# Performance work log

Hardware: AMD Instinct MI355X
Metric: run time of the kernel (lower is better)

Reference implementation:

```python
import jax, jax.numpy as jnp
import numpy as np

DIM = 2048; KV_RANK = 512; Q_RANK = 768; H = 16
D_NR = 128; D_R = 64; D_V = 128
B = 8; L = 32; MAX_T = 4096; START = MAX_T - L
QK_DIM = D_NR + D_R
SCALE = 1.0 / float(np.sqrt(QK_DIM))
EPS = 1.1920929e-07  # torch.finfo(float32).eps (nn.RMSNorm default)
ROPE_BASE = 10000.0


def rms_norm(x, w):
    return x * jax.lax.rsqrt(jnp.mean(x * x, axis=-1, keepdims=True) + EPS) * w


def apply_rope(x, cos, sin):
    # x: (b, l, h, d) with d even; cos/sin: (l, d//2) -> complex multiply on pairs
    b, l, h, d = x.shape
    xp = x.reshape(b, l, h, d // 2, 2)
    xr, xi = xp[..., 0], xp[..., 1]
    c = cos[None, :, None, :]
    s = sin[None, :, None, :]
    return jnp.stack([xr * c - xi * s, xr * s + xi * c], axis=-1).reshape(b, l, h, d)


def setup_inputs() -> dict:
    key = jax.random.key(0)
    ks = jax.random.split(key, 9)
    w = 0.02
    # rotary angles for absolute positions START..START+L-1
    inv_freq = 1.0 / (ROPE_BASE ** (np.arange(0, D_R, 2, dtype=np.float32) / D_R))  # (32,)
    pos = np.arange(START, START + L, dtype=np.float32)
    ang = pos[:, None] * inv_freq[None, :]  # (L, 32)
    # causal mask over full cache: query i sits at absolute position START+i
    t = jnp.arange(MAX_T)[None, :]
    qpos = START + jnp.arange(L)[:, None]
    mask = jnp.where(t <= qpos, 0.0, -1e30).astype(jnp.float32)  # (L, MAX_T)
    return {
        "x": jax.random.normal(ks[0], (B, L, DIM), dtype=jnp.float32),
        "start_pos": START,
        "freq_cos": jnp.asarray(np.cos(ang), dtype=jnp.float32),
        "freq_sin": jnp.asarray(np.sin(ang), dtype=jnp.float32),
        "mask": mask,
        "kv_latent_cache": jax.random.normal(ks[1], (B, MAX_T, KV_RANK), dtype=jnp.float32) * 0.05,
        "k_rope_cache": jax.random.normal(ks[2], (B, MAX_T, D_R), dtype=jnp.float32) * 0.05,
        "w_kv_down": jax.random.normal(ks[3], (KV_RANK + D_R, DIM), dtype=jnp.float32) * w,
        "w_q_down": jax.random.normal(ks[4], (Q_RANK, DIM), dtype=jnp.float32) * w,
        "rms_q_w": jnp.ones((Q_RANK,), dtype=jnp.float32),
        "w_q_up": jax.random.normal(ks[5], (H * QK_DIM, Q_RANK), dtype=jnp.float32) * w,
        "w_kv_up": jax.random.normal(ks[6], (H * (D_NR + D_V), KV_RANK), dtype=jnp.float32) * w,
        "w_out": jax.random.normal(ks[7], (DIM, H * D_V), dtype=jnp.float32) * w,
    }


def reference(x, start_pos, freq_cos, freq_sin, mask, kv_latent_cache, k_rope_cache,
              w_kv_down, w_q_down, rms_q_w, w_q_up, w_kv_up, w_out):
    b, l, _ = x.shape
    end_pos = start_pos + l
    # query path: down-proj -> RMSNorm -> up-proj (NOTE: module's rms_norm_kv is unused)
    q = rms_norm(x @ w_q_down.T, rms_q_w) @ w_q_up.T
    q = q.reshape(b, l, H, QK_DIM)
    q_nrope, q_rope = q[..., :D_NR], q[..., D_NR:]
    q_rope = apply_rope(q_rope, freq_cos, freq_sin)
    # latent kv path
    kv = x @ w_kv_down.T  # (b, l, KV_RANK + D_R)
    kv_latent, k_rope = kv[..., :KV_RANK], kv[..., KV_RANK:]
    k_rope = apply_rope(k_rope[:, :, None, :], freq_cos, freq_sin)[:, :, 0, :]
    # scatter-write into caches, then read prefix [:end_pos]
    kvc = kv_latent_cache.at[:, start_pos:end_pos].set(kv_latent)[:, :end_pos]  # (b, t, k)
    krc = k_rope_cache.at[:, start_pos:end_pos].set(k_rope)[:, :end_pos]        # (b, t, r)
    # weight absorption
    w_up = w_kv_up.reshape(H, D_NR + D_V, KV_RANK)
    q_abs = jnp.einsum('blhd,hdk->blhk', q_nrope, w_up[:, :D_NR])
    scores = (jnp.einsum('blhk,btk->blht', q_abs, kvc)
              + jnp.einsum('blhr,btr->blht', q_rope, krc)) * SCALE
    scores = scores + mask[None, :, None, :]
    p = jax.nn.softmax(scores, axis=-1)
    o = jnp.einsum('blht,btk->blhk', p, kvc)
    o = jnp.einsum('blhk,hdk->blhd', o, w_up[:, D_NR:])
    return o.reshape(b, l, H * D_V) @ w_out.T
```

## Files before the change

kernel.cpp:

```cpp
#include <hip/hip_runtime.h>
#include <math.h>

#define DIMX 2048
#define KV_RANK 512
#define Q_RANK 768
#define NH 16
#define D_NR 128
#define D_R 64
#define D_V 128
#define NB 8
#define NL 32
#define MAX_T 4096
#define STARTP (MAX_T - NL)
#define QK_DIM (D_NR + D_R)
#define ATT_SCALE 0.07216878364870323f
#define RMS_EPS 1.1920929e-07f

typedef unsigned short u16;
typedef __attribute__((ext_vector_type(4))) unsigned short u16x4;
typedef __attribute__((ext_vector_type(8))) short short8;
typedef __attribute__((ext_vector_type(4))) float f32x4;

#define GLOBAL_AS __attribute__((address_space(1)))
#define LDS_AS __attribute__((address_space(3)))

__device__ inline u16 f2b(float f) {
    union { float f; unsigned u; } v; v.f = f;
    unsigned r = (v.u + 0x7fffu + ((v.u >> 16) & 1u)) >> 16;
    return (u16)r;
}
__device__ inline float b2f(u16 u) {
    union { unsigned u; float f; } v; v.u = ((unsigned)u) << 16; return v.f;
}

template<int BM, int BN, bool OUTB, bool BSWZ>
__global__ __launch_bounds__(256) void gemm_mfma(
    const u16* __restrict__ A, const u16* __restrict__ B, void* __restrict__ Cv,
    int K, int lda, int ldb, int ldc,
    long long sA1, long long sA2, long long sB1, long long sB2,
    long long sC1, long long sC2, int nb2)
{
    constexpr int MFR = BM / 32;
    constexpr int NFR = BN / 32;
    int bx = blockIdx.x, by = blockIdx.y, bz = blockIdx.z;
    if (BSWZ) {
        int flat = bx + gridDim.x * (by + gridDim.y * bz);
        bz = flat & 7;
        int r = flat >> 3;
        bx = r % gridDim.x;
        by = r / gridDim.x;
    }
    const int z1 = bz / nb2, z2 = bz % nb2;
    A += z1 * sA1 + z2 * sA2;
    B += z1 * sB1 + z2 * sB2;

    const int m0 = by * BM;
    const int n0 = bx * BN;
    const int tid = threadIdx.x;
    const int lane = tid & 63;
    const int wid = tid >> 6;
    const int wm = wid >> 1, wn = wid & 1;
    const int l15 = lane & 15;
    const int l4  = lane >> 4;

    __shared__ __align__(16) u16 As[BM * 32];
    __shared__ __align__(16) u16 Bs[BN * 32];

    f32x4 acc[MFR][NFR];
    #pragma unroll
    for (int i = 0; i < MFR; ++i)
        #pragma unroll
        for (int j = 0; j < NFR; ++j)
            acc[i][j] = (f32x4)0.0f;

    constexpr int nA = BM / 16;
    constexpr int nB = BN / 16;

    for (int k0 = 0; k0 < K; k0 += 32) {
        #pragma unroll
        for (int j = 0; j < nA / 4 + 1; ++j) {
            int jj = wid + j * 4;
            if (jj < nA) {
                int c = jj * 64 + lane;
                const u16* src = A + (long long)(m0 + (c >> 2)) * lda + k0 + (c & 3) * 8;
                u16* dst = &As[jj * 512];
                __builtin_amdgcn_global_load_lds((const GLOBAL_AS void*)src,
                                                 (LDS_AS void*)dst, 16, 0, 0);
            }
        }
        #pragma unroll
        for (int j = 0; j < nB / 4 + 1; ++j) {
            int jj = wid + j * 4;
            if (jj < nB) {
                int c = jj * 64 + lane;
                const u16* src = B + (long long)(n0 + (c >> 2)) * ldb + k0 + (c & 3) * 8;
                u16* dst = &Bs[jj * 512];
                __builtin_amdgcn_global_load_lds((const GLOBAL_AS void*)src,
                                                 (LDS_AS void*)dst, 16, 0, 0);
            }
        }
        __syncthreads();

        short8 a[MFR], b[NFR];
        #pragma unroll
        for (int mf = 0; mf < MFR; ++mf)
            a[mf] = *(const short8*)&As[(wm * 16 * MFR + mf * 16 + l15) * 32 + l4 * 8];
        #pragma unroll
        for (int nf = 0; nf < NFR; ++nf)
            b[nf] = *(const short8*)&Bs[(wn * 16 * NFR + nf * 16 + l15) * 32 + l4 * 8];
        #pragma unroll
        for (int mf = 0; mf < MFR; ++mf)
            #pragma unroll
            for (int nf = 0; nf < NFR; ++nf)
                acc[mf][nf] = __builtin_amdgcn_mfma_f32_16x16x32_bf16(
                    a[mf], b[nf], acc[mf][nf], 0, 0, 0);
        __syncthreads();
    }

    if (OUTB) {
        u16* C = (u16*)Cv + z1 * sC1 + z2 * sC2;
        #pragma unroll
        for (int mf = 0; mf < MFR; ++mf)
            #pragma unroll
            for (int nf = 0; nf < NFR; ++nf) {
                int r0 = m0 + wm * 16 * MFR + mf * 16 + l4 * 4;
                int c0 = n0 + wn * 16 * NFR + nf * 16 + l15;
                #pragma unroll
                for (int r = 0; r < 4; ++r)
                    C[(long long)(r0 + r) * ldc + c0] = f2b(acc[mf][nf][r]);
            }
    } else {
        float* C = (float*)Cv + z1 * sC1 + z2 * sC2;
        #pragma unroll
        for (int mf = 0; mf < MFR; ++mf)
            #pragma unroll
            for (int nf = 0; nf < NFR; ++nf) {
                int r0 = m0 + wm * 16 * MFR + mf * 16 + l4 * 4;
                int c0 = n0 + wn * 16 * NFR + nf * 16 + l15;
                #pragma unroll
                for (int r = 0; r < 4; ++r)
                    C[(long long)(r0 + r) * ldc + c0] = acc[mf][nf][r];
            }
    }
}

struct Segs {
    const float* src[6];
    u16* dst[6];
    int n4[6];
};
__global__ __launch_bounds__(256) void f2b_multi(Segs s)
{
    int seg = blockIdx.y;
    int i = blockIdx.x * 256 + threadIdx.x;
    if (i >= s.n4[seg]) return;
    float4 v = ((const float4*)s.src[seg])[i];
    u16x4 o = { f2b(v.x), f2b(v.y), f2b(v.z), f2b(v.w) };
    ((u16x4*)s.dst[seg])[i] = o;
}

__global__ __launch_bounds__(256) void rms_reduce(const float* __restrict__ part,
                                                  const float* __restrict__ w,
                                                  u16* __restrict__ outb)
{
    const int row = blockIdx.x;
    const int tid = threadIdx.x;
    __shared__ float red[256];
    float val[3];
    float s = 0.f;
    #pragma unroll
    for (int j = 0; j < 3; ++j) {
        int i = tid + j * 256;
        long long off = (long long)row * Q_RANK + i;
        float v = part[off] + part[196608 + off] + part[393216 + off] + part[589824 + off];
        val[j] = v;
        s += v * v;
    }
    red[tid] = s; __syncthreads();
    for (int off = 128; off > 0; off >>= 1) {
        if (tid < off) red[tid] += red[tid + off];
        __syncthreads();
    }
    float scale = rsqrtf(red[0] / (float)Q_RANK + RMS_EPS);
    u16* ob = outb + (long long)row * Q_RANK;
    #pragma unroll
    for (int j = 0; j < 3; ++j) {
        int i = tid + j * 256;
        ob[i] = f2b(val[j] * scale * w[i]);
    }
}

__global__ __launch_bounds__(256) void wuT_kernel(const float* __restrict__ w,
                                                  u16* __restrict__ outp)
{
    __shared__ u16 T[64][65];
    const int h = blockIdx.z;
    const int y0 = blockIdx.y * 64;
    const int x0 = blockIdx.x * 64;
    const int tid = threadIdx.x;
    #pragma unroll
    for (int i = 0; i < 16; ++i) {
        int lin = i * 256 + tid;
        int r = lin >> 6, c = lin & 63;
        T[c][r] = f2b(w[((long long)h * 256 + y0 + r) * 512 + x0 + c]);
    }
    __syncthreads();
    #pragma unroll
    for (int i = 0; i < 16; ++i) {
        int lin = i * 256 + tid;
        int r = lin >> 6, c = lin & 63;
        outp[((long long)h * 512 + x0 + r) * 128 + y0 + c] = T[r][c];
    }
}

__global__ __launch_bounds__(256) void bcat_hist(const float* __restrict__ kvc,
                                                 const float* __restrict__ krc,
                                                 u16* __restrict__ bcat)
{
    int e = blockIdx.x * 256 + threadIdx.x;
    if (e >= NB * STARTP * 144) return;
    int c4 = e % 144;
    int row = e / 144;
    int b = row / STARTP, t = row % STARTP;
    float4 v;
    if (c4 < 128) v = ((const float4*)(kvc + ((long long)b * MAX_T + t) * KV_RANK))[c4];
    else          v = ((const float4*)(krc + ((long long)b * MAX_T + t) * D_R))[c4 - 128];
    u16x4 o = { f2b(v.x), f2b(v.y), f2b(v.z), f2b(v.w) };
    ((u16x4*)(bcat + ((long long)b * MAX_T + t) * 576))[c4] = o;
}

__global__ __launch_bounds__(256) void bcat_new_reduce(const float* __restrict__ part,
                                                       const float* __restrict__ fc,
                                                       const float* __restrict__ fs,
                                                       u16* __restrict__ bcat)
{
    const int bl = blockIdx.x;
    const int b = bl >> 5, l = bl & 31;
    const int t = threadIdx.x;
    if (t >= 144) return;
    long long off = (long long)bl * 576 + 4 * t;
    const float4* p0 = (const float4*)(part + off);
    float4 v0 = p0[0];
    float4 v1 = *(const float4*)(part + 147456 + off);
    float4 v2 = *(const float4*)(part + 294912 + off);
    float4 v3 = *(const float4*)(part + 442368 + off);
    float4 v = { v0.x + v1.x + v2.x + v3.x, v0.y + v1.y + v2.y + v3.y,
                 v0.z + v1.z + v2.z + v3.z, v0.w + v1.w + v2.w + v3.w };
    u16* dst = bcat + ((long long)b * MAX_T + STARTP + l) * 576;
    if (t < 128) {
        u16x4 o = { f2b(v.x), f2b(v.y), f2b(v.z), f2b(v.w) };
        ((u16x4*)dst)[t] = o;
    } else {
        int g = t - 128;
        float c0 = fc[l * 32 + 2 * g],     s0 = fs[l * 32 + 2 * g];
        float c1 = fc[l * 32 + 2 * g + 1], s1 = fs[l * 32 + 2 * g + 1];
        u16x4 o = { f2b(v.x * c0 - v.y * s0), f2b(v.x * s0 + v.y * c0),
                    f2b(v.z * c1 - v.w * s1), f2b(v.z * s1 + v.w * c1) };
        *(u16x4*)(dst + 512 + 4 * g) = o;
    }
}

__global__ __launch_bounds__(256) void t_kvcT(const u16* __restrict__ bcat,
                                              u16* __restrict__ kvcT)
{
    __shared__ u16 T[64][65];
    const int b = blockIdx.z;
    const int t0 = blockIdx.y * 64;
    const int k0 = blockIdx.x * 64;
    const int tid = threadIdx.x;
    const u16* in = bcat + ((long long)b * MAX_T + t0) * 576 + k0;
    #pragma unroll
    for (int i = 0; i < 16; ++i) {
        int lin = i * 256 + tid;
        int r = lin >> 6, c = lin & 63;
        T[c][r] = in[(long long)r * 576 + c];
    }
    __syncthreads();
    u16* outp = kvcT + ((long long)b * KV_RANK + k0) * MAX_T + t0;
    #pragma unroll
    for (int i = 0; i < 16; ++i) {
        int lin = i * 256 + tid;
        int r = lin >> 6, c = lin & 63;
        outp[(long long)r * MAX_T + c] = T[r][c];
    }
}

__global__ __launch_bounds__(256) void rope_q(const u16* __restrict__ qb,
                                              const float* __restrict__ fc,
                                              const float* __restrict__ fs,
                                              u16* __restrict__ qprimeb)
{
    int idx = blockIdx.x * 256 + threadIdx.x;
    int i = idx & 31;
    int h = (idx >> 5) & (NH - 1);
    int l = (idx >> 9) & (NL - 1);
    int b = idx >> 14;
    const u16* src = qb + (long long)(b * NL + l) * 3072 + h * QK_DIM + D_NR + 2 * i;
    float xr = b2f(src[0]), xi = b2f(src[1]);
    float c = fc[l * 32 + i], s = fs[l * 32 + i];
    u16* dst = qprimeb + ((long long)(b * NH + h) * NL + l) * 576 + 512 + 2 * i;
    dst[0] = f2b(xr * c - xi * s);
    dst[1] = f2b(xr * s + xi * c);
}

__global__ __launch_bounds__(256) void softmax_bf16(float* __restrict__ scores)
{
    const int row = blockIdx.x;
    const int l = row & 31;
    const int vlen = STARTP + l + 1;
    float* s = scores + (long long)row * MAX_T;
    __shared__ float red[256];
    const int tid = threadIdx.x;

    float4 v[4];
    float m = -1e30f;
    #pragma unroll
    for (int i = 0; i < 4; ++i) {
        int f4 = i * 256 + tid;
        v[i] = ((const float4*)s)[f4];
        int t = f4 * 4;
        if (t + 0 >= vlen) v[i].x = -1e30f;
        if (t + 1 >= vlen) v[i].y = -1e30f;
        if (t + 2 >= vlen) v[i].z = -1e30f;
        if (t + 3 >= vlen) v[i].w = -1e30f;
        m = fmaxf(m, fmaxf(fmaxf(v[i].x, v[i].y), fmaxf(v[i].z, v[i].w)));
    }
    red[tid] = m; __syncthreads();
    for (int off = 128; off > 0; off >>= 1) {
        if (tid < off) red[tid] = fmaxf(red[tid], red[tid + off]);
        __syncthreads();
    }
    const float mm = red[0] * ATT_SCALE;
    __syncthreads();

    float sum = 0.f;
    #pragma unroll
    for (int i = 0; i < 4; ++i) {
        v[i].x = __expf(v[i].x * ATT_SCALE - mm);
        v[i].y = __expf(v[i].y * ATT_SCALE - mm);
        v[i].z = __expf(v[i].z * ATT_SCALE - mm);
        v[i].w = __expf(v[i].w * ATT_SCALE - mm);
        sum += v[i].x + v[i].y + v[i].z + v[i].w;
    }
    red[tid] = sum; __syncthreads();
    for (int off = 128; off > 0; off >>= 1) {
        if (tid < off) red[tid] += red[tid + off];
        __syncthreads();
    }
    const float inv = 1.0f / red[0];
    u16* ps = (u16*)s;
    #pragma unroll
    for (int i = 0; i < 4; ++i) {
        int f4 = i * 256 + tid;
        u16x4 o = { f2b(v[i].x * inv), f2b(v[i].y * inv), f2b(v[i].z * inv), f2b(v[i].w * inv) };
        ((u16x4*)ps)[f4] = o;
    }
}

__global__ __launch_bounds__(256) void reduce_pv(const float* __restrict__ part,
                                                 u16* __restrict__ o_hb)
{
    int idx = blockIdx.x * 256 + threadIdx.x;
    int b = idx >> 16;
    int i4 = idx & 65535;
    const float* p = part + (long long)b * 1048576 + 4 * i4;
    float4 v0 = *(const float4*)p;
    float4 v1 = *(const float4*)(p + 262144);
    float4 v2 = *(const float4*)(p + 524288);
    float4 v3 = *(const float4*)(p + 786432);
    u16x4 o = { f2b(v0.x + v1.x + v2.x + v3.x), f2b(v0.y + v1.y + v2.y + v3.y),
                f2b(v0.z + v1.z + v2.z + v3.z), f2b(v0.w + v1.w + v2.w + v3.w) };
    ((u16x4*)(o_hb + (long long)b * 262144))[i4] = o;
}

__global__ __launch_bounds__(256) void reduce_out(const float* __restrict__ part,
                                                  float* __restrict__ out)
{
    int idx = blockIdx.x * 256 + threadIdx.x;
    const float* p = part + 4 * (long long)idx;
    float4 v0 = *(const float4*)p;
    float4 v1 = *(const float4*)(p + 524288);
    float4 v2 = *(const float4*)(p + 1048576);
    float4 v3 = *(const float4*)(p + 1572864);
    float4 o = { v0.x + v1.x + v2.x + v3.x, v0.y + v1.y + v2.y + v3.y,
                 v0.z + v1.z + v2.z + v3.z, v0.w + v1.w + v2.w + v3.w };
    ((float4*)out)[idx] = o;
}

extern "C" void kernel_launch(void* const* d_in, const int* in_sizes, int n_in,
                              void* d_out, int out_size, void* d_ws, size_t ws_size,
                              hipStream_t stream)
{
    const float* x        = (const float*)d_in[0];
    const float* fc       = (const float*)d_in[2];
    const float* fs       = (const float*)d_in[3];
    const float* kvc      = (const float*)d_in[5];
    const float* krc      = (const float*)d_in[6];
    const float* w_kv_down= (const float*)d_in[7];
    const float* w_q_down = (const float*)d_in[8];
    const float* rms_q_w  = (const float*)d_in[9];
    const float* w_q_up   = (const float*)d_in[10];
    const float* w_kv_up  = (const float*)d_in[11];
    const float* w_out    = (const float*)d_in[12];
    float* out            = (float*)d_out;

    float* qd_part = (float*)d_ws;
    float* kv_part = qd_part + 786432;
    float* scores  = kv_part + 589824;
    u16* base      = (u16*)(scores + 16777216);
    u16* xb      = base;                 base += 524288;
    u16* qdb     = base;                 base += 196608;
    u16* qb      = base;                 base += 786432;
    u16* qprimeb = base;                 base += 2359296;
    u16* wqd_b   = base;                 base += 1572864;
    u16* wqu_b   = base;                 base += 2359296;
    u16* wkvd_b  = base;                 base += 1179648;
    u16* wkvu_b  = base;                 base += 2097152;
    u16* wout_b  = base;                 base += 4194304;
    u16* wuT     = base;                 base += 1048576;
    u16* bcat    = base;                 base += 18874368;
    u16* kvcT    = base;                 base += 16777216;
    u16* o_hb    = base;                 base += 2097152;
    u16* o_upb   = base;                 base += 524288;
    float* pv_part  = (float*)bcat;
    float* out_part = (float*)kvcT;

    Segs segs;
    segs.src[0] = x;         segs.dst[0] = xb;     segs.n4[0] = 131072;
    segs.src[1] = w_q_down;  segs.dst[1] = wqd_b;  segs.n4[1] = 393216;
    segs.src[2] = w_q_up;    segs.dst[2] = wqu_b;  segs.n4[2] = 589824;
    segs.src[3] = w_kv_down; segs.dst[3] = wkvd_b; segs.n4[3] = 294912;
    segs.src[4] = w_kv_up;   segs.dst[4] = wkvu_b; segs.n4[4] = 524288;
    segs.src[5] = w_out;     segs.dst[5] = wout_b; segs.n4[5] = 1048576;
    f2b_multi<<<dim3(4096, 6), 256, 0, stream>>>(segs);

    wuT_kernel<<<dim3(8, 2, 16), 256, 0, stream>>>(w_kv_up, wuT);
    bcat_hist<<<(NB * STARTP * 144 + 255) / 256, 256, 0, stream>>>(kvc, krc, bcat);

    gemm_mfma<32, 64, false, false><<<dim3(12, 8, 4), 256, 0, stream>>>(
        xb, wqd_b, qd_part, 512, 2048, 2048, 768,
        0LL, 512LL, 0LL, 512LL, 0LL, 196608LL, 4);
    rms_reduce<<<256, 256, 0, stream>>>(qd_part, rms_q_w, qdb);
    gemm_mfma<32, 64, true, false><<<dim3(48, 8, 1), 256, 0, stream>>>(
        qdb, wqu_b, qb, 768, 768, 768, 3072, 0, 0, 0, 0, 0, 0, 1);
    gemm_mfma<32, 64, false, false><<<dim3(9, 8, 4), 256, 0, stream>>>(
        xb, wkvd_b, kv_part, 512, 2048, 2048, 576,
        0LL, 512LL, 0LL, 512LL, 0LL, 147456LL, 4);
    bcat_new_reduce<<<256, 256, 0, stream>>>(kv_part, fc, fs, bcat);
    t_kvcT<<<dim3(8, 64, 8), 256, 0, stream>>>(bcat, kvcT);

    gemm_mfma<32, 128, true, false><<<dim3(4, 1, 128), 256, 0, stream>>>(
        qb, wuT, qprimeb, 128, 3072, 128, 576,
        98304LL, 192LL, 0LL, 65536LL, 294912LL, 18432LL, 16);
    rope_q<<<512, 256, 0, stream>>>(qb, fc, fs, qprimeb);

    gemm_mfma<128, 128, false, true><<<dim3(32, 4, 8), 256, 0, stream>>>(
        qprimeb, bcat, scores, 576, 576, 576, 4096,
        294912LL, 0LL, 2359296LL, 0LL, 2097152LL, 0LL, 1);
    softmax_bf16<<<NB * NH * NL, 256, 0, stream>>>(scores);
    gemm_mfma<128, 128, false, false><<<dim3(4, 4, 32), 256, 0, stream>>>(
        (const u16*)scores, kvcT, pv_part, 1024, 8192, 4096, 512,
        4194304LL, 1024LL, 2097152LL, 1024LL, 1048576LL, 262144LL, 4);
    reduce_pv<<<2048, 256, 0, stream>>>(pv_part, o_hb);

    gemm_mfma<32, 64, true, false><<<dim3(2, 1, 128), 256, 0, stream>>>(
        o_hb, wkvu_b + 128 * 512, o_upb, 512, 512, 512, 2048,
        262144LL, 16384LL, 0LL, 131072LL, 65536LL, 128LL, 16);
    gemm_mfma<32, 64, false, false><<<dim3(32, 8, 4), 256, 0, stream>>>(
        o_upb, wout_b, out_part, 512, 2048, 2048, 2048,
        0LL, 512LL, 0LL, 512LL, 0LL, 524288LL, 4);
    reduce_out<<<512, 256, 0, stream>>>(out_part, out);
}
```

Before: 345.5 us.

## Merge q/kv down-projection GEMMs, fuse cache conversion with transpose, add XCD swizzle

```diff
diff --git a/kernel.cpp b/kernel.cpp
--- a/kernel.cpp
+++ b/kernel.cpp
@@ -24,6 +24,9 @@
 #define GLOBAL_AS __attribute__((address_space(1)))
 #define LDS_AS __attribute__((address_space(3)))
 
+#define NDOWN 1344
+#define DPART ((long long)256 * NDOWN)
+
 __device__ inline u16 f2b(float f) {
     union { float f; unsigned u; } v; v.f = f;
     unsigned r = (v.u + 0x7fffu + ((v.u >> 16) & 1u)) >> 16;
@@ -33,7 +36,7 @@
     union { unsigned u; float f; } v; v.u = ((unsigned)u) << 16; return v.f;
 }
 
-template<int BM, int BN, bool OUTB, bool BSWZ>
+template<int BM, int BN, bool OUTB, bool GSWZ>
 __global__ __launch_bounds__(256) void gemm_mfma(
     const u16* __restrict__ A, const u16* __restrict__ B, void* __restrict__ Cv,
     int K, int lda, int ldb, int ldc,
@@ -43,12 +46,14 @@
     constexpr int MFR = BM / 32;
     constexpr int NFR = BN / 32;
     int bx = blockIdx.x, by = blockIdx.y, bz = blockIdx.z;
-    if (BSWZ) {
+    if (GSWZ) {
         int flat = bx + gridDim.x * (by + gridDim.y * bz);
-        bz = flat & 7;
-        int r = flat >> 3;
-        bx = r % gridDim.x;
-        by = r / gridDim.x;
+        int nwg = gridDim.x * gridDim.y * gridDim.z;
+        int lf = (flat & 7) * (nwg >> 3) + (flat >> 3);
+        bx = lf % gridDim.x;
+        int r = lf / gridDim.x;
+        by = r % gridDim.y;
+        bz = r / gridDim.y;
     }
     const int z1 = bz / nb2, z2 = bz % nb2;
     A += z1 * sA1 + z2 * sA2;
@@ -171,8 +176,8 @@
     #pragma unroll
     for (int j = 0; j < 3; ++j) {
         int i = tid + j * 256;
-        long long off = (long long)row * Q_RANK + i;
-        float v = part[off] + part[196608 + off] + part[393216 + off] + part[589824 + off];
+        long long off = (long long)row * NDOWN + i;
+        float v = part[off] + part[DPART + off] + part[2 * DPART + off] + part[3 * DPART + off];
         val[j] = v;
         s += v * v;
     }
@@ -213,20 +218,17 @@
     }
 }
 
-__global__ __launch_bounds__(256) void bcat_hist(const float* __restrict__ kvc,
-                                                 const float* __restrict__ krc,
-                                                 u16* __restrict__ bcat)
+__global__ __launch_bounds__(256) void bcat_rope_hist(const float* __restrict__ krc,
+                                                      u16* __restrict__ bcat)
 {
     int e = blockIdx.x * 256 + threadIdx.x;
-    if (e >= NB * STARTP * 144) return;
-    int c4 = e % 144;
-    int row = e / 144;
-    int b = row / STARTP, t = row % STARTP;
-    float4 v;
-    if (c4 < 128) v = ((const float4*)(kvc + ((long long)b * MAX_T + t) * KV_RANK))[c4];
-    else          v = ((const float4*)(krc + ((long long)b * MAX_T + t) * D_R))[c4 - 128];
+    if (e >= NB * STARTP * 16) return;
+    int c4 = e & 15;
+    int row = e >> 4;
+    int b = row / STARTP, t = row - b * STARTP;
+    float4 v = ((const float4*)(krc + ((long long)b * MAX_T + t) * D_R))[c4];
     u16x4 o = { f2b(v.x), f2b(v.y), f2b(v.z), f2b(v.w) };
-    ((u16x4*)(bcat + ((long long)b * MAX_T + t) * 576))[c4] = o;
+    ((u16x4*)(bcat + ((long long)b * MAX_T + t) * 576 + 512))[c4] = o;
 }
 
 __global__ __launch_bounds__(256) void bcat_new_reduce(const float* __restrict__ part,
@@ -238,12 +240,11 @@
     const int b = bl >> 5, l = bl & 31;
     const int t = threadIdx.x;
     if (t >= 144) return;
-    long long off = (long long)bl * 576 + 4 * t;
-    const float4* p0 = (const float4*)(part + off);
-    float4 v0 = p0[0];
-    float4 v1 = *(const float4*)(part + 147456 + off);
-    float4 v2 = *(const float4*)(part + 294912 + off);
-    float4 v3 = *(const float4*)(part + 442368 + off);
+    long long off = (long long)bl * NDOWN + 768 + 4 * t;
+    float4 v0 = *(const float4*)(part + off);
+    float4 v1 = *(const float4*)(part + DPART + off);
+    float4 v2 = *(const float4*)(part + 2 * DPART + off);
+    float4 v3 = *(const float4*)(part + 3 * DPART + off);
     float4 v = { v0.x + v1.x + v2.x + v3.x, v0.y + v1.y + v2.y + v3.y,
                  v0.z + v1.z + v2.z + v3.z, v0.w + v1.w + v2.w + v3.w };
     u16* dst = bcat + ((long long)b * MAX_T + STARTP + l) * 576;
@@ -260,20 +261,28 @@
     }
 }
 
-__global__ __launch_bounds__(256) void t_kvcT(const u16* __restrict__ bcat,
-                                              u16* __restrict__ kvcT)
+__global__ __launch_bounds__(256) void prep_cache(const float* __restrict__ kvc,
+                                                  u16* __restrict__ bcat,
+                                                  u16* __restrict__ kvcT)
 {
     __shared__ u16 T[64][65];
     const int b = blockIdx.z;
     const int t0 = blockIdx.y * 64;
     const int k0 = blockIdx.x * 64;
     const int tid = threadIdx.x;
-    const u16* in = bcat + ((long long)b * MAX_T + t0) * 576 + k0;
     #pragma unroll
     for (int i = 0; i < 16; ++i) {
         int lin = i * 256 + tid;
         int r = lin >> 6, c = lin & 63;
-        T[c][r] = in[(long long)r * 576 + c];
+        int t = t0 + r;
+        u16 v;
+        if (t < STARTP) {
+            v = f2b(kvc[((long long)b * MAX_T + t) * KV_RANK + k0 + c]);
+            bcat[((long long)b * MAX_T + t) * 576 + k0 + c] = v;
+        } else {
+            v = bcat[((long long)b * MAX_T + t) * 576 + k0 + c];
+        }
+        T[c][r] = v;
     }
     __syncthreads();
     u16* outp = kvcT + ((long long)b * KV_RANK + k0) * MAX_T + t0;
@@ -404,17 +413,15 @@
     const float* w_out    = (const float*)d_in[12];
     float* out            = (float*)d_out;
 
-    float* qd_part = (float*)d_ws;
-    float* kv_part = qd_part + 786432;
-    float* scores  = kv_part + 589824;
+    float* down_part = (float*)d_ws;
+    float* scores  = down_part + 1376256;
     u16* base      = (u16*)(scores + 16777216);
     u16* xb      = base;                 base += 524288;
     u16* qdb     = base;                 base += 196608;
     u16* qb      = base;                 base += 786432;
     u16* qprimeb = base;                 base += 2359296;
-    u16* wqd_b   = base;                 base += 1572864;
+    u16* wqkv_b  = base;                 base += 2752512;
     u16* wqu_b   = base;                 base += 2359296;
-    u16* wkvd_b  = base;                 base += 1179648;
     u16* wkvu_b  = base;                 base += 2097152;
     u16* wout_b  = base;                 base += 4194304;
     u16* wuT     = base;                 base += 1048576;
@@ -426,30 +433,27 @@
     float* out_part = (float*)kvcT;
 
     Segs segs;
-    segs.src[0] = x;         segs.dst[0] = xb;     segs.n4[0] = 131072;
-    segs.src[1] = w_q_down;  segs.dst[1] = wqd_b;  segs.n4[1] = 393216;
-    segs.src[2] = w_q_up;    segs.dst[2] = wqu_b;  segs.n4[2] = 589824;
-    segs.src[3] = w_kv_down; segs.dst[3] = wkvd_b; segs.n4[3] = 294912;
-    segs.src[4] = w_kv_up;   segs.dst[4] = wkvu_b; segs.n4[4] = 524288;
-    segs.src[5] = w_out;     segs.dst[5] = wout_b; segs.n4[5] = 1048576;
+    segs.src[0] = x;         segs.dst[0] = xb;                  segs.n4[0] = 131072;
+    segs.src[1] = w_q_down;  segs.dst[1] = wqkv_b;              segs.n4[1] = 393216;
+    segs.src[2] = w_q_up;    segs.dst[2] = wqu_b;               segs.n4[2] = 589824;
+    segs.src[3] = w_kv_down; segs.dst[3] = wqkv_b + 768 * 2048; segs.n4[3] = 294912;
+    segs.src[4] = w_kv_up;   segs.dst[4] = wkvu_b;              segs.n4[4] = 524288;
+    segs.src[5] = w_out;     segs.dst[5] = wout_b;              segs.n4[5] = 1048576;
     f2b_multi<<<dim3(4096, 6), 256, 0, stream>>>(segs);
 
     wuT_kernel<<<dim3(8, 2, 16), 256, 0, stream>>>(w_kv_up, wuT);
-    bcat_hist<<<(NB * STARTP * 144 + 255) / 256, 256, 0, stream>>>(kvc, krc, bcat);
-
-    gemm_mfma<32, 64, false, false><<<dim3(12, 8, 4), 256, 0, stream>>>(
-        xb, wqd_b, qd_part, 512, 2048, 2048, 768,
-        0LL, 512LL, 0LL, 512LL, 0LL, 196608LL, 4);
-    rms_reduce<<<256, 256, 0, stream>>>(qd_part, rms_q_w, qdb);
-    gemm_mfma<32, 64, true, false><<<dim3(48, 8, 1), 256, 0, stream>>>(
+    bcat_rope_hist<<<(NB * STARTP * 16 + 255) / 256, 256, 0, stream>>>(krc, bcat);
+
+    gemm_mfma<32, 64, false, true><<<dim3(21, 8, 4), 256, 0, stream>>>(
+        xb, wqkv_b, down_part, 512, 2048, 2048, NDOWN,
+        0LL, 512LL, 0LL, 512LL, 0LL, DPART, 4);
+    rms_reduce<<<256, 256, 0, stream>>>(down_part, rms_q_w, qdb);
+    gemm_mfma<32, 64, true, true><<<dim3(48, 8, 1), 256, 0, stream>>>(
         qdb, wqu_b, qb, 768, 768, 768, 3072, 0, 0, 0, 0, 0, 0, 1);
-    gemm_mfma<32, 64, false, false><<<dim3(9, 8, 4), 256, 0, stream>>>(
-        xb, wkvd_b, kv_part, 512, 2048, 2048, 576,
-        0LL, 512LL, 0LL, 512LL, 0LL, 147456LL, 4);
-    bcat_new_reduce<<<256, 256, 0, stream>>>(kv_part, fc, fs, bcat);
-    t_kvcT<<<dim3(8, 64, 8), 256, 0, stream>>>(bcat, kvcT);
-
-    gemm_mfma<32, 128, true, false><<<dim3(4, 1, 128), 256, 0, stream>>>(
+    bcat_new_reduce<<<256, 256, 0, stream>>>(down_part, fc, fs, bcat);
+    prep_cache<<<dim3(8, 64, 8), 256, 0, stream>>>(kvc, bcat, kvcT);
+
+    gemm_mfma<32, 128, true, true><<<dim3(4, 1, 128), 256, 0, stream>>>(
         qb, wuT, qprimeb, 128, 3072, 128, 576,
         98304LL, 192LL, 0LL, 65536LL, 294912LL, 18432LL, 16);
     rope_q<<<512, 256, 0, stream>>>(qb, fc, fs, qprimeb);
@@ -458,15 +462,15 @@
         qprimeb, bcat, scores, 576, 576, 576, 4096,
         294912LL, 0LL, 2359296LL, 0LL, 2097152LL, 0LL, 1);
     softmax_bf16<<<NB * NH * NL, 256, 0, stream>>>(scores);
-    gemm_mfma<128, 128, false, false><<<dim3(4, 4, 32), 256, 0, stream>>>(
+    gemm_mfma<128, 128, false, true><<<dim3(4, 4, 32), 256, 0, stream>>>(
         (const u16*)scores, kvcT, pv_part, 1024, 8192, 4096, 512,
         4194304LL, 1024LL, 2097152LL, 1024LL, 1048576LL, 262144LL, 4);
     reduce_pv<<<2048, 256, 0, stream>>>(pv_part, o_hb);
 
-    gemm_mfma<32, 64, true, false><<<dim3(2, 1, 128), 256, 0, stream>>>(
+    gemm_mfma<32, 64, true, true><<<dim3(2, 1, 128), 256, 0, stream>>>(
         o_hb, wkvu_b + 128 * 512, o_upb, 512, 512, 512, 2048,
         262144LL, 16384LL, 0LL, 131072LL, 65536LL, 128LL, 16);
-    gemm_mfma<32, 64, false, false><<<dim3(32, 8, 4), 256, 0, stream>>>(
+    gemm_mfma<32, 64, false, true><<<dim3(32, 8, 4), 256, 0, stream>>>(
         o_upb, wout_b, out_part, 512, 2048, 2048, 2048,
         0LL, 512LL, 0LL, 512LL, 0LL, 524288LL, 4);
     reduce_out<<<512, 256, 0, stream>>>(out_part, out);
```

Result: no change. 339.0 us (-1.9%).
